# Kernel optimization log

Hardware: AMD Instinct MI355X
Metric: run time of the kernel (lower is better)

Reference implementation:

```python
import jax, jax.numpy as jnp
import numpy as np

MARGIN = 0.3


def setup_inputs() -> dict:
    key = jax.random.key(0)
    k1, k2 = jax.random.split(key)
    inputs = jax.random.normal(k1, (8192, 256), dtype=jnp.float32)
    targets = jax.random.randint(k2, (8192,), 0, 512, dtype=jnp.int64)
    return {"inputs": inputs, "targets": targets}


def reference(inputs, targets):
    # L2-normalize features (normalize_feature=True default)
    x = inputs / (jnp.linalg.norm(inputs, axis=-1, keepdims=True) + 1e-12)
    n = x.shape[0]
    # pairwise euclidean distance [n, n]
    sq = jnp.sum(x * x, axis=1)
    dist = sq[:, None] + sq[None, :] - 2.0 * (x @ x.T)
    dist = jnp.sqrt(jnp.clip(dist, 1e-12, None))
    # positive / negative masks
    same = targets[:, None] == targets[None, :]
    eye = jnp.eye(n, dtype=bool)
    is_same = same & ~eye          # positives, diagonal excluded
    is_diff = ~same                # negatives
    neg_inf = jnp.float32(-jnp.inf)
    pos_inf = jnp.float32(jnp.inf)
    # hard positive: max over positives per row (fallback 0.0 if none)
    dist_ap = jnp.max(jnp.where(is_same, dist, neg_inf), axis=1)
    dist_ap = jnp.where(jnp.any(is_same, axis=1), dist_ap, 0.0)
    # hard negative: min over negatives per row (fallback margin+1 if none)
    dist_an = jnp.min(jnp.where(is_diff, dist, pos_inf), axis=1)
    dist_an = jnp.where(jnp.any(is_diff, axis=1), dist_an, MARGIN + 1.0)
    # MarginRankingLoss with y=1: mean(max(0, -(an - ap) + margin))
    loss = jnp.mean(jnp.maximum(0.0, dist_ap - dist_an + MARGIN))
    return loss
```

## Files before the change

kernel.cpp:

```cpp
#include <hip/hip_runtime.h>
#include <hip/hip_bf16.h>

#define NROWS  8192
#define DIM    256
#define NCLASS 512
#define MARGIN 0.3f

using bf16x8 = __attribute__((ext_vector_type(8))) short;
using f32x4  = __attribute__((ext_vector_type(4))) float;

__device__ inline ushort f2bf(float f) {
    __hip_bfloat16 h = __float2bfloat16(f);
    return *reinterpret_cast<ushort*>(&h);
}
__device__ inline float bf2f(ushort u) {
    return __uint_as_float(((unsigned)u) << 16);
}
__device__ inline unsigned f2ord(float f) {
    unsigned b = __float_as_uint(f);
    return (b & 0x80000000u) ? ~b : (b | 0x80000000u);
}
__device__ inline float ord2f(unsigned u) {
    return __uint_as_float((u & 0x80000000u) ? (u & 0x7FFFFFFFu) : ~u);
}
__device__ inline void ld16_g2l(const void* g, void* l) {
    __builtin_amdgcn_global_load_lds(
        (const __attribute__((address_space(1))) unsigned int*)g,
        (__attribute__((address_space(3))) unsigned int*)l, 16, 0, 0);
}

#define XBS_OFF 0u
#define SQS_OFF 4194304u
#define TGT_OFF 4227072u
#define PMX_OFF 4259840u
#define NMN_OFF 4292608u
#define BIN_OFF 4325376u
#define ACC_OFF 4327424u
#define TIK_OFF 4327432u

__global__ __launch_bounds__(512) void hist_scan_kernel(
    const int* __restrict__ tgt, int* __restrict__ bincur,
    double* __restrict__ accd, unsigned* __restrict__ ticket)
{
    __shared__ int h[NCLASS];
    int tid = threadIdx.x;
    h[tid] = 0;
    if (tid == 0) { *accd = 0.0; *ticket = 0u; }
    __syncthreads();
    for (int k = 0; k < NROWS / NCLASS; ++k)
        atomicAdd(&h[tgt[tid + k * NCLASS]], 1);
    __syncthreads();
    int cnt = h[tid];
    for (int ofs = 1; ofs < NCLASS; ofs <<= 1) {
        int v = (tid >= ofs) ? h[tid - ofs] : 0;
        __syncthreads();
        h[tid] += v;
        __syncthreads();
    }
    bincur[tid] = h[tid] - cnt;
}

__global__ __launch_bounds__(256) void norm_scatter_kernel(
    const float* __restrict__ in, const int* __restrict__ tgt,
    int* __restrict__ bincur, ushort* __restrict__ xbs,
    float* __restrict__ sqs, int* __restrict__ tgts,
    unsigned* __restrict__ pmax, unsigned* __restrict__ nmin)
{
    int row  = blockIdx.x * 4 + (threadIdx.x >> 6);
    int lane = threadIdx.x & 63;
    float4 v = ((const float4*)(in + (size_t)row * DIM))[lane];
    float ss = v.x * v.x + v.y * v.y + v.z * v.z + v.w * v.w;
#pragma unroll
    for (int m = 1; m < 64; m <<= 1) ss += __shfl_xor(ss, m, 64);
    float inv = 1.0f / (sqrtf(ss) + 1e-12f);

    ushort4 st;
    st.x = f2bf(v.x * inv); st.y = f2bf(v.y * inv);
    st.z = f2bf(v.z * inv); st.w = f2bf(v.w * inv);

    int t = 0, dst = 0;
    if (lane == 0) { t = tgt[row]; dst = atomicAdd(&bincur[t], 1); }
    dst = __shfl(dst, 0); t = __shfl(t, 0);

    ((ushort4*)(xbs + (size_t)dst * DIM))[lane] = st;

    float a0 = bf2f(st.x), a1 = bf2f(st.y), a2 = bf2f(st.z), a3 = bf2f(st.w);
    float s2 = a0 * a0 + a1 * a1 + a2 * a2 + a3 * a3;
#pragma unroll
    for (int m = 1; m < 64; m <<= 1) s2 += __shfl_xor(s2, m, 64);
    if (lane == 0) {
        sqs[dst]  = s2;
        tgts[dst] = t;
        pmax[dst] = 0x007FFFFFu;
        nmin[dst] = 0xFF800000u;
    }
}

__global__ __launch_bounds__(256, 2) void gram_kernel(
    const ushort* __restrict__ xbs, const float* __restrict__ sqs,
    const int* __restrict__ tgts, unsigned* __restrict__ pmax,
    unsigned* __restrict__ nmin)
{
    __shared__ struct {
        char  buf[2][16384];
        float sqc[512];
        int   tgc[512];
        int   tga[256];
    } sm;

    const int wave = threadIdx.x >> 6;
    const int lane = threadIdx.x & 63;
    const int l15  = lane & 15;
    const int quad = lane >> 4;
    const int mbase = blockIdx.x * 256 + wave * 64;
    const int nbase = blockIdx.y * 512;

    {
        int c = threadIdx.x * 2;
        sm.sqc[c]     = sqs[nbase + c];
        sm.sqc[c + 1] = sqs[nbase + c + 1];
        sm.tgc[c]     = tgts[nbase + c];
        sm.tgc[c + 1] = tgts[nbase + c + 1];
        sm.tga[threadIdx.x] = tgts[blockIdx.x * 256 + threadIdx.x];
    }

    bf16x8 afrag[4][8];
#pragma unroll
    for (int a = 0; a < 4; ++a) {
        const ushort* arow = xbs + (size_t)(mbase + a * 16 + l15) * DIM + quad * 8;
#pragma unroll
        for (int kk = 0; kk < 8; ++kk)
            afrag[a][kk] = *(const bf16x8*)(arow + kk * 32);
    }
    const int rlo = tgts[mbase];
    const int rhi = tgts[mbase + 63];

    const int colh = lane >> 5, c31 = lane & 31;
    int offs[4];
#pragma unroll
    for (int j = 0; j < 4; ++j)
        offs[j] = colh * 512 + ((c31 ^ ((2 * j + colh) & 7)) << 4);

    const char* xbs_b = (const char*)xbs;

    {
        const char* gbase = xbs_b + (size_t)nbase * 512;
#pragma unroll
        for (int j = 0; j < 4; ++j) {
            int i = wave * 4 + j;
            ld16_g2l(gbase + i * 1024 + offs[j], sm.buf[0] + i * 1024);
        }
    }
    __syncthreads();

    float pm[16], nm[16];
#pragma unroll
    for (int j = 0; j < 16; ++j) { pm[j] = -__builtin_inff(); nm[j] = __builtin_inff(); }

#pragma unroll 2
    for (int s = 0; s < 16; ++s) {
        if (s < 15) {
            const char* gbase = xbs_b + (size_t)(nbase + (s + 1) * 32) * 512;
            char* lbase = sm.buf[(s + 1) & 1];
#pragma unroll
            for (int j = 0; j < 4; ++j) {
                int i = wave * 4 + j;
                ld16_g2l(gbase + i * 1024 + offs[j], lbase + i * 1024);
            }
        }
        const char* bufc = sm.buf[s & 1];
#pragma unroll
        for (int u = 0; u < 2; ++u) {
            const int t16 = s * 32 + u * 16;
            bf16x8 bfrag[8];
#pragma unroll
            for (int kk = 0; kk < 8; ++kk)
                bfrag[kk] = *(const bf16x8*)(bufc + u * 8192 + l15 * 512 +
                                             (((quad + 4 * kk) ^ (l15 & 7)) << 4));
            f32x4 acc4[4];
#pragma unroll
            for (int a = 0; a < 4; ++a) {
                f32x4 acc = {0.f, 0.f, 0.f, 0.f};
#pragma unroll
                for (int kk = 0; kk < 8; ++kk)
                    acc = __builtin_amdgcn_mfma_f32_16x16x32_bf16(afrag[a][kk], bfrag[kk], acc, 0, 0, 0);
                acc4[a] = acc;
            }
            const float sqc = sm.sqc[t16 + l15];
            const int clo = sm.tgc[t16], chi = sm.tgc[t16 + 15];
            if (rlo <= chi && clo <= rhi) {
                const int tc = sm.tgc[t16 + l15];
#pragma unroll
                for (int a = 0; a < 4; ++a)
#pragma unroll
                    for (int i = 0; i < 4; ++i) {
                        const float v = fmaf(acc4[a][i], -2.0f, sqc);
                        const bool same = (sm.tga[wave * 64 + a * 16 + quad * 4 + i] == tc);
                        pm[a * 4 + i] = fmaxf(pm[a * 4 + i], same ? v : -__builtin_inff());
                        nm[a * 4 + i] = fminf(nm[a * 4 + i], same ? __builtin_inff() : v);
                    }
            } else {
#pragma unroll
                for (int a = 0; a < 4; ++a)
#pragma unroll
                    for (int i = 0; i < 4; ++i)
                        nm[a * 4 + i] = fminf(nm[a * 4 + i], fmaf(acc4[a][i], -2.0f, sqc));
            }
        }
        __syncthreads();
    }

#pragma unroll
    for (int m = 1; m < 16; m <<= 1) {
#pragma unroll
        for (int j = 0; j < 16; ++j) {
            pm[j] = fmaxf(pm[j], __shfl_xor(pm[j], m, 64));
            nm[j] = fminf(nm[j], __shfl_xor(nm[j], m, 64));
        }
    }
    if (l15 == 0) {
#pragma unroll
        for (int a = 0; a < 4; ++a)
#pragma unroll
            for (int i = 0; i < 4; ++i) {
                int r = mbase + a * 16 + quad * 4 + i;
                atomicMax(&pmax[r], f2ord(pm[a * 4 + i]));
                atomicMin(&nmin[r], f2ord(nm[a * 4 + i]));
            }
    }
}

__global__ __launch_bounds__(256) void finalize_kernel(
    const unsigned* __restrict__ pmax, const unsigned* __restrict__ nmin,
    const float* __restrict__ sqs, double* __restrict__ accd,
    unsigned* __restrict__ ticket, float* __restrict__ out)
{
    int r = blockIdx.x * 256 + threadIdx.x;
    float pe = ord2f(pmax[r]);
    float ne = ord2f(nmin[r]);
    float ap = sqrtf(fmaxf(sqs[r] + pe, 0.0f));
    float an = (ne > 1e30f) ? (MARGIN + 1.0f) : sqrtf(fmaxf(sqs[r] + ne, 0.0f));
    float h  = fmaxf(ap - an + MARGIN, 0.0f);
    double s = (double)h;
#pragma unroll
    for (int m = 1; m < 64; m <<= 1) s += __shfl_xor(s, m, 64);
    __shared__ double sh[4];
    if ((threadIdx.x & 63) == 0) sh[threadIdx.x >> 6] = s;
    __syncthreads();
    if (threadIdx.x == 0) {
        double b = sh[0] + sh[1] + sh[2] + sh[3];
        atomicAdd(accd, b);
        __threadfence();
        unsigned old = atomicAdd(ticket, 1u);
        if (old == gridDim.x - 1) {
            double total = atomicAdd(accd, 0.0);
            out[0] = (float)(total / (double)NROWS);
        }
    }
}

extern "C" void kernel_launch(void* const* d_in, const int* in_sizes, int n_in,
                              void* d_out, int out_size, void* d_ws, size_t ws_size,
                              hipStream_t stream) {
    const float* in  = (const float*)d_in[0];
    const int*   tgt = (const int*)d_in[1];
    float*       out = (float*)d_out;

    char* ws = (char*)d_ws;
    ushort*   xbs    = (ushort*)(ws + XBS_OFF);
    float*    sqs    = (float*)(ws + SQS_OFF);
    int*      tgts   = (int*)(ws + TGT_OFF);
    unsigned* pmax   = (unsigned*)(ws + PMX_OFF);
    unsigned* nmin   = (unsigned*)(ws + NMN_OFF);
    int*      bincur = (int*)(ws + BIN_OFF);
    double*   accd   = (double*)(ws + ACC_OFF);
    unsigned* ticket = (unsigned*)(ws + TIK_OFF);

    hist_scan_kernel<<<1, 512, 0, stream>>>(tgt, bincur, accd, ticket);
    norm_scatter_kernel<<<NROWS / 4, 256, 0, stream>>>(in, tgt, bincur, xbs, sqs, tgts, pmax, nmin);
    gram_kernel<<<dim3(32, 16), 256, 0, stream>>>(xbs, sqs, tgts, pmax, nmin);
    finalize_kernel<<<32, 256, 0, stream>>>(pmax, nmin, sqs, accd, ticket, out);
}
```

Measured before the change: 114.9 us.

## Fuse histogram scan into normalize-scatter kernel with per-block redundant prefix sums

Removes the single-block histogram/scan launch. Each of 512 prep blocks now recomputes the full class histogram and prefix sum in shared memory, then normalizes and scatters 16 rows using a global per-class counter zeroed by a memset. The accumulator and ticket are reset by that same memset. This trades one serial single-block kernel and its launch gap for redundant per-block histogram work over all 8192 targets and an extra memset.

```diff
diff --git a/kernel.cpp b/kernel.cpp
--- a/kernel.cpp
+++ b/kernel.cpp
@@ -34,65 +34,72 @@
 #define TGT_OFF 4227072u
 #define PMX_OFF 4259840u
 #define NMN_OFF 4292608u
-#define BIN_OFF 4325376u
+#define CNT_OFF 4325376u
 #define ACC_OFF 4327424u
 #define TIK_OFF 4327432u
 
-__global__ __launch_bounds__(512) void hist_scan_kernel(
-    const int* __restrict__ tgt, int* __restrict__ bincur,
-    double* __restrict__ accd, unsigned* __restrict__ ticket)
-{
-    __shared__ int h[NCLASS];
-    int tid = threadIdx.x;
-    h[tid] = 0;
-    if (tid == 0) { *accd = 0.0; *ticket = 0u; }
-    __syncthreads();
-    for (int k = 0; k < NROWS / NCLASS; ++k)
-        atomicAdd(&h[tgt[tid + k * NCLASS]], 1);
-    __syncthreads();
-    int cnt = h[tid];
-    for (int ofs = 1; ofs < NCLASS; ofs <<= 1) {
-        int v = (tid >= ofs) ? h[tid - ofs] : 0;
-        __syncthreads();
-        h[tid] += v;
-        __syncthreads();
-    }
-    bincur[tid] = h[tid] - cnt;
-}
-
-__global__ __launch_bounds__(256) void norm_scatter_kernel(
+__global__ __launch_bounds__(256) void prep_kernel(
     const float* __restrict__ in, const int* __restrict__ tgt,
-    int* __restrict__ bincur, ushort* __restrict__ xbs,
+    int* __restrict__ cnt2, ushort* __restrict__ xbs,
     float* __restrict__ sqs, int* __restrict__ tgts,
     unsigned* __restrict__ pmax, unsigned* __restrict__ nmin)
 {
-    int row  = blockIdx.x * 4 + (threadIdx.x >> 6);
-    int lane = threadIdx.x & 63;
-    float4 v = ((const float4*)(in + (size_t)row * DIM))[lane];
-    float ss = v.x * v.x + v.y * v.y + v.z * v.z + v.w * v.w;
-#pragma unroll
-    for (int m = 1; m < 64; m <<= 1) ss += __shfl_xor(ss, m, 64);
-    float inv = 1.0f / (sqrtf(ss) + 1e-12f);
-
-    ushort4 st;
-    st.x = f2bf(v.x * inv); st.y = f2bf(v.y * inv);
-    st.z = f2bf(v.z * inv); st.w = f2bf(v.w * inv);
-
-    int t = 0, dst = 0;
-    if (lane == 0) { t = tgt[row]; dst = atomicAdd(&bincur[t], 1); }
-    dst = __shfl(dst, 0); t = __shfl(t, 0);
-
-    ((ushort4*)(xbs + (size_t)dst * DIM))[lane] = st;
-
-    float a0 = bf2f(st.x), a1 = bf2f(st.y), a2 = bf2f(st.z), a3 = bf2f(st.w);
-    float s2 = a0 * a0 + a1 * a1 + a2 * a2 + a3 * a3;
-#pragma unroll
-    for (int m = 1; m < 64; m <<= 1) s2 += __shfl_xor(s2, m, 64);
-    if (lane == 0) {
-        sqs[dst]  = s2;
-        tgts[dst] = t;
-        pmax[dst] = 0x007FFFFFu;
-        nmin[dst] = 0xFF800000u;
+    __shared__ int hcnt[NCLASS];
+    __shared__ int h[NCLASS];
+    const int b   = blockIdx.x;
+    const int tid = threadIdx.x;
+
+    hcnt[tid] = 0; hcnt[tid + 256] = 0;
+    __syncthreads();
+#pragma unroll 4
+    for (int k = 0; k < NROWS / 256; ++k)
+        atomicAdd(&hcnt[tgt[tid + k * 256]], 1);
+    __syncthreads();
+    h[tid] = hcnt[tid]; h[tid + 256] = hcnt[tid + 256];
+    __syncthreads();
+    for (int ofs = 1; ofs < NCLASS; ofs <<= 1) {
+        int v0 = (tid >= ofs) ? h[tid - ofs] : 0;
+        int v1 = (tid + 256 >= ofs) ? h[tid + 256 - ofs] : 0;
+        __syncthreads();
+        h[tid]       += v0;
+        h[tid + 256] += v1;
+        __syncthreads();
+    }
+
+    const int wv   = tid >> 6;
+    const int lane = tid & 63;
+#pragma unroll 1
+    for (int rr = 0; rr < 4; ++rr) {
+        int row = b * 16 + wv * 4 + rr;
+        float4 v = ((const float4*)(in + (size_t)row * DIM))[lane];
+        float ss = v.x * v.x + v.y * v.y + v.z * v.z + v.w * v.w;
+#pragma unroll
+        for (int m = 1; m < 64; m <<= 1) ss += __shfl_xor(ss, m, 64);
+        float inv = 1.0f / (sqrtf(ss) + 1e-12f);
+
+        ushort4 st;
+        st.x = f2bf(v.x * inv); st.y = f2bf(v.y * inv);
+        st.z = f2bf(v.z * inv); st.w = f2bf(v.w * inv);
+
+        int t = 0, dst = 0;
+        if (lane == 0) {
+            t = tgt[row];
+            dst = (h[t] - hcnt[t]) + atomicAdd(&cnt2[t], 1);
+        }
+        dst = __shfl(dst, 0); t = __shfl(t, 0);
+
+        ((ushort4*)(xbs + (size_t)dst * DIM))[lane] = st;
+
+        float a0 = bf2f(st.x), a1 = bf2f(st.y), a2 = bf2f(st.z), a3 = bf2f(st.w);
+        float s2 = a0 * a0 + a1 * a1 + a2 * a2 + a3 * a3;
+#pragma unroll
+        for (int m = 1; m < 64; m <<= 1) s2 += __shfl_xor(s2, m, 64);
+        if (lane == 0) {
+            sqs[dst]  = s2;
+            tgts[dst] = t;
+            pmax[dst] = 0x007FFFFFu;
+            nmin[dst] = 0xFF800000u;
+        }
     }
 }
 
@@ -272,12 +279,12 @@
     int*      tgts   = (int*)(ws + TGT_OFF);
     unsigned* pmax   = (unsigned*)(ws + PMX_OFF);
     unsigned* nmin   = (unsigned*)(ws + NMN_OFF);
-    int*      bincur = (int*)(ws + BIN_OFF);
+    int*      cnt2   = (int*)(ws + CNT_OFF);
     double*   accd   = (double*)(ws + ACC_OFF);
     unsigned* ticket = (unsigned*)(ws + TIK_OFF);
 
-    hist_scan_kernel<<<1, 512, 0, stream>>>(tgt, bincur, accd, ticket);
-    norm_scatter_kernel<<<NROWS / 4, 256, 0, stream>>>(in, tgt, bincur, xbs, sqs, tgts, pmax, nmin);
+    hipMemsetAsync(ws + CNT_OFF, 0, 2060, stream);
+    prep_kernel<<<512, 256, 0, stream>>>(in, tgt, cnt2, xbs, sqs, tgts, pmax, nmin);
     gram_kernel<<<dim3(32, 16), 256, 0, stream>>>(xbs, sqs, tgts, pmax, nmin);
     finalize_kernel<<<32, 256, 0, stream>>>(pmax, nmin, sqs, accd, ticket, out);
 }
```

Result: slower. 122.3 us (+6.5%).

## Drop class-sorting prepass and always apply same-class masking in gram tiles

Applied to the files above, without the earlier changes.

Removes the single-block histogram/prefix-scan kernel and the atomic scatter that reordered rows by class. The normalize kernel now writes rows in place and also initializes the accumulator and ticket. The gram kernel reads the original targets directly and runs the full same/different comparison on every tile, instead of skipping the positive check for tiles whose sorted class ranges cannot overlap. This saves one serial launch and the scatter atomics, but adds per-element LDS target loads and compare/select work to every tile's epilogue.

```diff
diff --git a/kernel.cpp b/kernel.cpp
--- a/kernel.cpp
+++ b/kernel.cpp
@@ -3,7 +3,6 @@
 
 #define NROWS  8192
 #define DIM    256
-#define NCLASS 512
 #define MARGIN 0.3f
 
 using bf16x8 = __attribute__((ext_vector_type(8))) short;
@@ -31,43 +30,20 @@
 
 #define XBS_OFF 0u
 #define SQS_OFF 4194304u
-#define TGT_OFF 4227072u
 #define PMX_OFF 4259840u
 #define NMN_OFF 4292608u
-#define BIN_OFF 4325376u
 #define ACC_OFF 4327424u
 #define TIK_OFF 4327432u
 
-__global__ __launch_bounds__(512) void hist_scan_kernel(
-    const int* __restrict__ tgt, int* __restrict__ bincur,
-    double* __restrict__ accd, unsigned* __restrict__ ticket)
-{
-    __shared__ int h[NCLASS];
-    int tid = threadIdx.x;
-    h[tid] = 0;
-    if (tid == 0) { *accd = 0.0; *ticket = 0u; }
-    __syncthreads();
-    for (int k = 0; k < NROWS / NCLASS; ++k)
-        atomicAdd(&h[tgt[tid + k * NCLASS]], 1);
-    __syncthreads();
-    int cnt = h[tid];
-    for (int ofs = 1; ofs < NCLASS; ofs <<= 1) {
-        int v = (tid >= ofs) ? h[tid - ofs] : 0;
-        __syncthreads();
-        h[tid] += v;
-        __syncthreads();
-    }
-    bincur[tid] = h[tid] - cnt;
-}
-
-__global__ __launch_bounds__(256) void norm_scatter_kernel(
-    const float* __restrict__ in, const int* __restrict__ tgt,
-    int* __restrict__ bincur, ushort* __restrict__ xbs,
-    float* __restrict__ sqs, int* __restrict__ tgts,
-    unsigned* __restrict__ pmax, unsigned* __restrict__ nmin)
+__global__ __launch_bounds__(256) void norm_kernel(
+    const float* __restrict__ in, ushort* __restrict__ xbs,
+    float* __restrict__ sqs, unsigned* __restrict__ pmax,
+    unsigned* __restrict__ nmin, double* __restrict__ accd,
+    unsigned* __restrict__ ticket)
 {
     int row  = blockIdx.x * 4 + (threadIdx.x >> 6);
     int lane = threadIdx.x & 63;
+    if (blockIdx.x == 0 && threadIdx.x == 0) { *accd = 0.0; *ticket = 0u; }
     float4 v = ((const float4*)(in + (size_t)row * DIM))[lane];
     float ss = v.x * v.x + v.y * v.y + v.z * v.z + v.w * v.w;
 #pragma unroll
@@ -78,27 +54,22 @@
     st.x = f2bf(v.x * inv); st.y = f2bf(v.y * inv);
     st.z = f2bf(v.z * inv); st.w = f2bf(v.w * inv);
 
-    int t = 0, dst = 0;
-    if (lane == 0) { t = tgt[row]; dst = atomicAdd(&bincur[t], 1); }
-    dst = __shfl(dst, 0); t = __shfl(t, 0);
-
-    ((ushort4*)(xbs + (size_t)dst * DIM))[lane] = st;
+    ((ushort4*)(xbs + (size_t)row * DIM))[lane] = st;
 
     float a0 = bf2f(st.x), a1 = bf2f(st.y), a2 = bf2f(st.z), a3 = bf2f(st.w);
     float s2 = a0 * a0 + a1 * a1 + a2 * a2 + a3 * a3;
 #pragma unroll
     for (int m = 1; m < 64; m <<= 1) s2 += __shfl_xor(s2, m, 64);
     if (lane == 0) {
-        sqs[dst]  = s2;
-        tgts[dst] = t;
-        pmax[dst] = 0x007FFFFFu;
-        nmin[dst] = 0xFF800000u;
+        sqs[row]  = s2;
+        pmax[row] = 0x007FFFFFu;
+        nmin[row] = 0xFF800000u;
     }
 }
 
 __global__ __launch_bounds__(256, 2) void gram_kernel(
     const ushort* __restrict__ xbs, const float* __restrict__ sqs,
-    const int* __restrict__ tgts, unsigned* __restrict__ pmax,
+    const int* __restrict__ tgt, unsigned* __restrict__ pmax,
     unsigned* __restrict__ nmin)
 {
     __shared__ struct {
@@ -119,9 +90,9 @@
         int c = threadIdx.x * 2;
         sm.sqc[c]     = sqs[nbase + c];
         sm.sqc[c + 1] = sqs[nbase + c + 1];
-        sm.tgc[c]     = tgts[nbase + c];
-        sm.tgc[c + 1] = tgts[nbase + c + 1];
-        sm.tga[threadIdx.x] = tgts[blockIdx.x * 256 + threadIdx.x];
+        sm.tgc[c]     = tgt[nbase + c];
+        sm.tgc[c + 1] = tgt[nbase + c + 1];
+        sm.tga[threadIdx.x] = tgt[blockIdx.x * 256 + threadIdx.x];
     }
 
     bf16x8 afrag[4][8];
@@ -132,8 +103,6 @@
         for (int kk = 0; kk < 8; ++kk)
             afrag[a][kk] = *(const bf16x8*)(arow + kk * 32);
     }
-    const int rlo = tgts[mbase];
-    const int rhi = tgts[mbase + 63];
 
     const int colh = lane >> 5, c31 = lane & 31;
     int offs[4];
@@ -187,25 +156,16 @@
                 acc4[a] = acc;
             }
             const float sqc = sm.sqc[t16 + l15];
-            const int clo = sm.tgc[t16], chi = sm.tgc[t16 + 15];
-            if (rlo <= chi && clo <= rhi) {
-                const int tc = sm.tgc[t16 + l15];
-#pragma unroll
-                for (int a = 0; a < 4; ++a)
-#pragma unroll
-                    for (int i = 0; i < 4; ++i) {
-                        const float v = fmaf(acc4[a][i], -2.0f, sqc);
-                        const bool same = (sm.tga[wave * 64 + a * 16 + quad * 4 + i] == tc);
-                        pm[a * 4 + i] = fmaxf(pm[a * 4 + i], same ? v : -__builtin_inff());
-                        nm[a * 4 + i] = fminf(nm[a * 4 + i], same ? __builtin_inff() : v);
-                    }
-            } else {
-#pragma unroll
-                for (int a = 0; a < 4; ++a)
-#pragma unroll
-                    for (int i = 0; i < 4; ++i)
-                        nm[a * 4 + i] = fminf(nm[a * 4 + i], fmaf(acc4[a][i], -2.0f, sqc));
-            }
+            const int   tc  = sm.tgc[t16 + l15];
+#pragma unroll
+            for (int a = 0; a < 4; ++a)
+#pragma unroll
+                for (int i = 0; i < 4; ++i) {
+                    const float v = fmaf(acc4[a][i], -2.0f, sqc);
+                    const bool same = (sm.tga[wave * 64 + a * 16 + quad * 4 + i] == tc);
+                    pm[a * 4 + i] = fmaxf(pm[a * 4 + i], same ? v : -__builtin_inff());
+                    nm[a * 4 + i] = fminf(nm[a * 4 + i], same ? __builtin_inff() : v);
+                }
         }
         __syncthreads();
     }
@@ -269,15 +229,12 @@
     char* ws = (char*)d_ws;
     ushort*   xbs    = (ushort*)(ws + XBS_OFF);
     float*    sqs    = (float*)(ws + SQS_OFF);
-    int*      tgts   = (int*)(ws + TGT_OFF);
     unsigned* pmax   = (unsigned*)(ws + PMX_OFF);
     unsigned* nmin   = (unsigned*)(ws + NMN_OFF);
-    int*      bincur = (int*)(ws + BIN_OFF);
     double*   accd   = (double*)(ws + ACC_OFF);
     unsigned* ticket = (unsigned*)(ws + TIK_OFF);
 
-    hist_scan_kernel<<<1, 512, 0, stream>>>(tgt, bincur, accd, ticket);
-    norm_scatter_kernel<<<NROWS / 4, 256, 0, stream>>>(in, tgt, bincur, xbs, sqs, tgts, pmax, nmin);
-    gram_kernel<<<dim3(32, 16), 256, 0, stream>>>(xbs, sqs, tgts, pmax, nmin);
+    norm_kernel<<<NROWS / 4, 256, 0, stream>>>(in, xbs, sqs, pmax, nmin, accd, ticket);
+    gram_kernel<<<dim3(32, 16), 256, 0, stream>>>(xbs, sqs, tgt, pmax, nmin);
     finalize_kernel<<<32, 256, 0, stream>>>(pmax, nmin, sqs, accd, ticket, out);
 }
```

Result: faster. 108.3 us, median of 3 (-5.7%).
